# Performance work log

Measured on AMD Instinct MI355X. Metric: run time of the kernel, lower is better.

## Reference

```python
import jax, jax.numpy as jnp
import numpy as np

DELTA_VAR = 0.5
DELTA_DIST = 1.5
LOSS_WEIGHT = 1.0
L_MAX = 17  # segment ids 0..16 (0 = background)
EPS = 1e-12


def setup_inputs() -> dict:
    key = jax.random.key(0)
    k1, k2 = jax.random.split(key)
    B, D, H, W = 16, 16, 288, 512
    emb = jax.random.normal(k1, (B, D, H, W), dtype=jnp.float32)
    seg = jax.random.randint(k2, (B, 1, H, W), 0, L_MAX, dtype=jnp.int64)
    return {"input": emb, "target": seg}


def _per_image_losses(e, s):
    # e: [D, N] float, s: [N] int labels in [0, L_MAX)
    D, N = e.shape
    et = e.T  # [N, D]
    cnt = jax.ops.segment_sum(jnp.ones((N,), e.dtype), s, num_segments=L_MAX)  # [L]
    sums = jax.ops.segment_sum(et, s, num_segments=L_MAX)                      # [L, D]
    present = (cnt > 0) & (jnp.arange(L_MAX) != 0)
    num_lanes = jnp.sum(present).astype(e.dtype)
    means = sums / jnp.maximum(cnt, 1.0)[:, None]                              # [L, D]

    # variance (pull) term: per-pixel distance to own-label centroid
    diff = et - means[s]                                                       # [N, D]
    nrm = jnp.sqrt(jnp.maximum(jnp.sum(diff * diff, axis=1), EPS))             # [N]
    term = jax.nn.relu(nrm - DELTA_VAR) ** 2
    per_label = jax.ops.segment_sum(term, s, num_segments=L_MAX) / jnp.maximum(cnt, 1.0)
    var_l = jnp.sum(jnp.where(present, per_label, 0.0)) / jnp.maximum(num_lanes, 1.0)
    var_l = jnp.where(num_lanes > 0, var_l, 0.0)

    # distance (push) term: pairwise centroid distances among present lanes
    d = means[:, None, :] - means[None, :, :]                                  # [L, L, D]
    sumsq = jnp.sum(d * d, axis=2)                                             # [L, L]
    pair_mask = present[:, None] & present[None, :] & ~jnp.eye(L_MAX, dtype=bool)
    dist = jnp.sqrt(jnp.where(pair_mask, sumsq, 1.0))
    push = jnp.sum(jnp.where(pair_mask, jax.nn.relu(DELTA_DIST - dist) ** 2, 0.0))
    denom = jnp.maximum(num_lanes * (num_lanes - 1.0), 1.0)
    dist_l = jnp.where(num_lanes > 1, push / denom / 2.0, 0.0)
    return var_l, dist_l


def reference(input, target):
    B, D, H, W = input.shape
    N = H * W
    emb = input.reshape(B, D, N)
    seg = target.reshape(B, N).astype(jnp.int32)
    var_l, dist_l = jax.vmap(_per_image_losses)(emb, seg)
    loss = (jnp.sum(var_l) + jnp.sum(dist_l)) / B
    return loss * LOSS_WEIGHT
```

## Files before the change

### kernel.cpp

```cpp
#include <hip/hip_runtime.h>

#define BB   16
#define DD   16
#define NN   (288*512)
#define LL   17
#define TPB  256
#define PB   96
#define PXB  (NN/PB)
#define TILE 512
#define PBV  144
#define NREP 16

#define FSCALE 32768.0f
#define INV_FSCALE (1.0f/32768.0f)


__global__ __launch_bounds__(TPB) void k_accum(const float* __restrict__ emb,
                                               const int* __restrict__ seg,
                                               int* __restrict__ acc) {
    __shared__ int slab[TILE];
    __shared__ int tab[NREP * 289];
    const int tid  = threadIdx.x;
    const int b    = blockIdx.y;
    const int blk  = blockIdx.x;
    const int dgrp = tid >> 6;
    const int j    = tid & 63;
    int* trep = tab + (j & (NREP - 1)) * 289;

    for (int i = tid; i < NREP * 289; i += TPB) tab[i] = 0;

    const float* embb = emb + (size_t)b * DD * NN;
    const int*   segb = seg + (size_t)b * NN;
    const int base0 = blk * PXB;
    const float* r0 = embb + (size_t)(dgrp * 4 + 0) * NN;
    const float* r1 = embb + (size_t)(dgrp * 4 + 1) * NN;
    const float* r2 = embb + (size_t)(dgrp * 4 + 2) * NN;
    const float* r3 = embb + (size_t)(dgrp * 4 + 3) * NN;
    __syncthreads();

    for (int t = 0; t < PXB / TILE; ++t) {
        const int tb = base0 + t * TILE;
        if (tid < TILE / 4)
            *(int4*)(slab + tid * 4) = *(const int4*)(segb + tb + tid * 4);
        __syncthreads();
#pragma unroll
        for (int s = 0; s < TILE / 256; ++s) {
            const int p = s * 256 + j * 4;
            const int4   s4 = *(const int4*)(slab + p);
            const float4 e0 = *(const float4*)(r0 + tb + p);
            const float4 e1 = *(const float4*)(r1 + tb + p);
            const float4 e2 = *(const float4*)(r2 + tb + p);
            const float4 e3 = *(const float4*)(r3 + tb + p);
            const int o0 = s4.x * 17 + dgrp * 4;
            const int o1 = s4.y * 17 + dgrp * 4;
            const int o2 = s4.z * 17 + dgrp * 4;
            const int o3 = s4.w * 17 + dgrp * 4;
            atomicAdd(trep + o0 + 0, __float2int_rn(e0.x * FSCALE));
            atomicAdd(trep + o0 + 1, __float2int_rn(e1.x * FSCALE));
            atomicAdd(trep + o0 + 2, __float2int_rn(e2.x * FSCALE));
            atomicAdd(trep + o0 + 3, __float2int_rn(e3.x * FSCALE));
            atomicAdd(trep + o1 + 0, __float2int_rn(e0.y * FSCALE));
            atomicAdd(trep + o1 + 1, __float2int_rn(e1.y * FSCALE));
            atomicAdd(trep + o1 + 2, __float2int_rn(e2.y * FSCALE));
            atomicAdd(trep + o1 + 3, __float2int_rn(e3.y * FSCALE));
            atomicAdd(trep + o2 + 0, __float2int_rn(e0.z * FSCALE));
            atomicAdd(trep + o2 + 1, __float2int_rn(e1.z * FSCALE));
            atomicAdd(trep + o2 + 2, __float2int_rn(e2.z * FSCALE));
            atomicAdd(trep + o2 + 3, __float2int_rn(e3.z * FSCALE));
            atomicAdd(trep + o3 + 0, __float2int_rn(e0.w * FSCALE));
            atomicAdd(trep + o3 + 1, __float2int_rn(e1.w * FSCALE));
            atomicAdd(trep + o3 + 2, __float2int_rn(e2.w * FSCALE));
            atomicAdd(trep + o3 + 3, __float2int_rn(e3.w * FSCALE));
            if (dgrp == 0) {
                atomicAdd(trep + s4.x * 17 + 16, 1);
                atomicAdd(trep + s4.y * 17 + 16, 1);
                atomicAdd(trep + s4.z * 17 + 16, 1);
                atomicAdd(trep + s4.w * 17 + 16, 1);
            }
        }
        __syncthreads();
    }

    for (int i = tid; i < 289; i += TPB) {
        int v = 0;
#pragma unroll
        for (int r = 0; r < NREP; ++r) v += tab[r * 289 + i];
        atomicAdd(acc + b * 289 + i, v);
    }
}

__global__ __launch_bounds__(64) void k_stats(const int* __restrict__ acc,
                                              float* __restrict__ gmean,
                                              float* __restrict__ gw,
                                              float* __restrict__ dvec) {
    __shared__ float mm[289];
    const int tid = threadIdx.x;
    const int b = blockIdx.x;
    for (int i = tid; i < 289; i += 64) {
        const int raw = acc[b * 289 + i];
        mm[i] = (i % 17 == 16) ? (float)raw : (float)raw * INV_FSCALE;
    }
    __syncthreads();
    for (int i = tid; i < 272; i += 64) {
        const int l = i >> 4, d = i & 15;
        const float c = mm[l * 17 + 16];
        const float mv = mm[l * 17 + d] / fmaxf(c, 1.f);
        mm[l * 17 + d] = mv;
        gmean[(size_t)b * 272 + i] = mv;
    }
    __syncthreads();

    int nl = 0;
#pragma unroll
    for (int l = 1; l < LL; ++l) nl += (mm[l * 17 + 16] > 0.f) ? 1 : 0;
    const float nlf = (float)nl;

    if (tid < LL) {
        const bool pres = (tid != 0) && (mm[tid * 17 + 16] > 0.f);
        gw[(size_t)b * 17 + tid] = pres
            ? 1.f / (fmaxf(mm[tid * 17 + 16], 1.f) * fmaxf(nlf, 1.f) * (float)BB) : 0.f;
    }

    float push = 0.f;
    for (int p = tid; p < 289; p += 64) {
        const int i = p / 17, jj = p % 17;
        if (i != jj && i > 0 && jj > 0 && mm[i*17+16] > 0.f && mm[jj*17+16] > 0.f) {
            float ss = 0.f;
#pragma unroll
            for (int d = 0; d < DD; ++d) {
                const float df = mm[i*17+d] - mm[jj*17+d];
                ss += df * df;
            }
            const float t = fmaxf(1.5f - sqrtf(ss), 0.f);
            push += t * t;
        }
    }
#pragma unroll
    for (int off = 32; off; off >>= 1) push += __shfl_down(push, off, 64);
    if (tid == 0)
        dvec[b] = (nl > 1) ? push / (fmaxf(nlf * (nlf - 1.f), 1.f) * 2.f * (float)BB) : 0.f;
}

__global__ __launch_bounds__(TPB) void k_var(const float* __restrict__ emb,
                                             const int* __restrict__ seg,
                                             const float* __restrict__ gmean,
                                             const float* __restrict__ gw,
                                             float* __restrict__ vpart) {
    __shared__ float m[289];
    __shared__ float wl[17];
    __shared__ float wsum[TPB / 64];
    const int tid = threadIdx.x;
    const int b = blockIdx.y;
    for (int i = tid; i < 272; i += TPB)
        m[(i >> 4) * 17 + (i & 15)] = gmean[(size_t)b * 272 + i];
    if (tid < LL) wl[tid] = gw[(size_t)b * 17 + tid];
    __syncthreads();

    const float* embb = emb + (size_t)b * DD * NN;
    const int*   segb = seg + (size_t)b * NN;

    const int n = blockIdx.x * (TPB * 4) + tid * 4;
    const int4 s4 = *(const int4*)(segb + n);
    const int o0 = s4.x * 17, o1 = s4.y * 17, o2 = s4.z * 17, o3 = s4.w * 17;
    float ss0 = 0.f, ss1 = 0.f, ss2 = 0.f, ss3 = 0.f;
#pragma unroll
    for (int d = 0; d < DD; ++d) {
        const float4 e = *(const float4*)(embb + (size_t)d * NN + n);
        const float d0 = e.x - m[o0 + d]; ss0 += d0 * d0;
        const float d1 = e.y - m[o1 + d]; ss1 += d1 * d1;
        const float d2 = e.z - m[o2 + d]; ss2 += d2 * d2;
        const float d3 = e.w - m[o3 + d]; ss3 += d3 * d3;
    }
    float accl = 0.f, t;
    t = fmaxf(sqrtf(fmaxf(ss0, 1e-12f)) - 0.5f, 0.f); accl += t * t * wl[s4.x];
    t = fmaxf(sqrtf(fmaxf(ss1, 1e-12f)) - 0.5f, 0.f); accl += t * t * wl[s4.y];
    t = fmaxf(sqrtf(fmaxf(ss2, 1e-12f)) - 0.5f, 0.f); accl += t * t * wl[s4.z];
    t = fmaxf(sqrtf(fmaxf(ss3, 1e-12f)) - 0.5f, 0.f); accl += t * t * wl[s4.w];

#pragma unroll
    for (int off = 32; off; off >>= 1) accl += __shfl_down(accl, off, 64);
    if ((tid & 63) == 0) wsum[tid >> 6] = accl;
    __syncthreads();
    if (tid == 0)
        vpart[(size_t)b * PBV + blockIdx.x] = wsum[0] + wsum[1] + wsum[2] + wsum[3];
}

__global__ __launch_bounds__(TPB) void k_final(const float* __restrict__ vpart,
                                               const float* __restrict__ dvec,
                                               float* __restrict__ out) {
    __shared__ float ws4[TPB / 64];
    float v = 0.f;
    for (int i = threadIdx.x; i < BB * PBV; i += TPB) v += vpart[i];
    if (threadIdx.x < BB) v += dvec[threadIdx.x];
#pragma unroll
    for (int off = 32; off; off >>= 1) v += __shfl_down(v, off, 64);
    if ((threadIdx.x & 63) == 0) ws4[threadIdx.x >> 6] = v;
    __syncthreads();
    if (threadIdx.x == 0) out[0] = ws4[0] + ws4[1] + ws4[2] + ws4[3];
}

extern "C" void kernel_launch(void* const* d_in, const int* in_sizes, int n_in,
                              void* d_out, int out_size, void* d_ws, size_t ws_size,
                              hipStream_t stream) {
    const float* emb = (const float*)d_in[0];
    const int*   seg = (const int*)d_in[1];
    float* out = (float*)d_out;

    int*   acc   = (int*)d_ws;
    float* gmean = (float*)(acc + BB * 289);
    float* gw    = gmean + BB * 272;
    float* dvec  = gw + BB * 17;
    float* vpart = dvec + BB;

    hipMemsetAsync(acc, 0, (size_t)BB * 289 * sizeof(int), stream);

    k_accum<<<dim3(PB, BB), TPB, 0, stream>>>(emb, seg, acc);
    k_stats<<<BB, 64, 0, stream>>>(acc, gmean, gw, dvec);
    k_var  <<<dim3(PBV, BB), TPB, 0, stream>>>(emb, seg, gmean, gw, vpart);
    k_final<<<1, TPB, 0, stream>>>(vpart, dvec, out);
}
```

Measured before the change: 252.4 us.

## Fold stats kernel into variance kernel and drop shared seg staging

Removes the separate k_stats launch: each k_var block now recomputes the means and per-label weights from the integer accumulators, and block 0 of each image also computes the push term. k_accum loads segment labels straight from global memory instead of staging them in a shared slab, which removes the per-tile barriers. The shared replica count drops from 16 to 8. This cuts one launch and its serial dependency, at the cost of redundant per-block setup work and more LDS atomic contention with fewer replicas.

```diff
diff --git a/kernel.cpp b/kernel.cpp
--- a/kernel.cpp
+++ b/kernel.cpp
@@ -6,10 +6,9 @@
 #define LL   17
 #define TPB  256
 #define PB   96
-#define PXB  (NN/PB)
-#define TILE 512
+#define QB   (NN/4/PB)
 #define PBV  144
-#define NREP 16
+#define NREP 8
 
 #define FSCALE 32768.0f
 #define INV_FSCALE (1.0f/32768.0f)
@@ -18,7 +17,6 @@
 __global__ __launch_bounds__(TPB) void k_accum(const float* __restrict__ emb,
                                                const int* __restrict__ seg,
                                                int* __restrict__ acc) {
-    __shared__ int slab[TILE];
     __shared__ int tab[NREP * 289];
     const int tid  = threadIdx.x;
     const int b    = blockIdx.y;
@@ -31,55 +29,50 @@
 
     const float* embb = emb + (size_t)b * DD * NN;
     const int*   segb = seg + (size_t)b * NN;
-    const int base0 = blk * PXB;
     const float* r0 = embb + (size_t)(dgrp * 4 + 0) * NN;
     const float* r1 = embb + (size_t)(dgrp * 4 + 1) * NN;
     const float* r2 = embb + (size_t)(dgrp * 4 + 2) * NN;
     const float* r3 = embb + (size_t)(dgrp * 4 + 3) * NN;
+    const int q0 = blk * QB;
     __syncthreads();
 
-    for (int t = 0; t < PXB / TILE; ++t) {
-        const int tb = base0 + t * TILE;
-        if (tid < TILE / 4)
-            *(int4*)(slab + tid * 4) = *(const int4*)(segb + tb + tid * 4);
-        __syncthreads();
 #pragma unroll
-        for (int s = 0; s < TILE / 256; ++s) {
-            const int p = s * 256 + j * 4;
-            const int4   s4 = *(const int4*)(slab + p);
-            const float4 e0 = *(const float4*)(r0 + tb + p);
-            const float4 e1 = *(const float4*)(r1 + tb + p);
-            const float4 e2 = *(const float4*)(r2 + tb + p);
-            const float4 e3 = *(const float4*)(r3 + tb + p);
-            const int o0 = s4.x * 17 + dgrp * 4;
-            const int o1 = s4.y * 17 + dgrp * 4;
-            const int o2 = s4.z * 17 + dgrp * 4;
-            const int o3 = s4.w * 17 + dgrp * 4;
-            atomicAdd(trep + o0 + 0, __float2int_rn(e0.x * FSCALE));
-            atomicAdd(trep + o0 + 1, __float2int_rn(e1.x * FSCALE));
-            atomicAdd(trep + o0 + 2, __float2int_rn(e2.x * FSCALE));
-            atomicAdd(trep + o0 + 3, __float2int_rn(e3.x * FSCALE));
-            atomicAdd(trep + o1 + 0, __float2int_rn(e0.y * FSCALE));
-            atomicAdd(trep + o1 + 1, __float2int_rn(e1.y * FSCALE));
-            atomicAdd(trep + o1 + 2, __float2int_rn(e2.y * FSCALE));
-            atomicAdd(trep + o1 + 3, __float2int_rn(e3.y * FSCALE));
-            atomicAdd(trep + o2 + 0, __float2int_rn(e0.z * FSCALE));
-            atomicAdd(trep + o2 + 1, __float2int_rn(e1.z * FSCALE));
-            atomicAdd(trep + o2 + 2, __float2int_rn(e2.z * FSCALE));
-            atomicAdd(trep + o2 + 3, __float2int_rn(e3.z * FSCALE));
-            atomicAdd(trep + o3 + 0, __float2int_rn(e0.w * FSCALE));
-            atomicAdd(trep + o3 + 1, __float2int_rn(e1.w * FSCALE));
-            atomicAdd(trep + o3 + 2, __float2int_rn(e2.w * FSCALE));
-            atomicAdd(trep + o3 + 3, __float2int_rn(e3.w * FSCALE));
-            if (dgrp == 0) {
-                atomicAdd(trep + s4.x * 17 + 16, 1);
-                atomicAdd(trep + s4.y * 17 + 16, 1);
-                atomicAdd(trep + s4.z * 17 + 16, 1);
-                atomicAdd(trep + s4.w * 17 + 16, 1);
-            }
+    for (int it = 0; it < QB / 64; ++it) {
+        const int n = (q0 + it * 64 + j) * 4;
+        const int4   s4 = *(const int4*)(segb + n);
+        const float4 e0 = *(const float4*)(r0 + n);
+        const float4 e1 = *(const float4*)(r1 + n);
+        const float4 e2 = *(const float4*)(r2 + n);
+        const float4 e3 = *(const float4*)(r3 + n);
+        const int ch = dgrp * 4;
+        const int o0 = s4.x * 17 + ch;
+        const int o1 = s4.y * 17 + ch;
+        const int o2 = s4.z * 17 + ch;
+        const int o3 = s4.w * 17 + ch;
+        atomicAdd(trep + o0 + 0, __float2int_rn(e0.x * FSCALE));
+        atomicAdd(trep + o0 + 1, __float2int_rn(e1.x * FSCALE));
+        atomicAdd(trep + o0 + 2, __float2int_rn(e2.x * FSCALE));
+        atomicAdd(trep + o0 + 3, __float2int_rn(e3.x * FSCALE));
+        atomicAdd(trep + o1 + 0, __float2int_rn(e0.y * FSCALE));
+        atomicAdd(trep + o1 + 1, __float2int_rn(e1.y * FSCALE));
+        atomicAdd(trep + o1 + 2, __float2int_rn(e2.y * FSCALE));
+        atomicAdd(trep + o1 + 3, __float2int_rn(e3.y * FSCALE));
+        atomicAdd(trep + o2 + 0, __float2int_rn(e0.z * FSCALE));
+        atomicAdd(trep + o2 + 1, __float2int_rn(e1.z * FSCALE));
+        atomicAdd(trep + o2 + 2, __float2int_rn(e2.z * FSCALE));
+        atomicAdd(trep + o2 + 3, __float2int_rn(e3.z * FSCALE));
+        atomicAdd(trep + o3 + 0, __float2int_rn(e0.w * FSCALE));
+        atomicAdd(trep + o3 + 1, __float2int_rn(e1.w * FSCALE));
+        atomicAdd(trep + o3 + 2, __float2int_rn(e2.w * FSCALE));
+        atomicAdd(trep + o3 + 3, __float2int_rn(e3.w * FSCALE));
+        if (dgrp == 0) {
+            atomicAdd(trep + s4.x * 17 + 16, 1);
+            atomicAdd(trep + s4.y * 17 + 16, 1);
+            atomicAdd(trep + s4.z * 17 + 16, 1);
+            atomicAdd(trep + s4.w * 17 + 16, 1);
         }
-        __syncthreads();
     }
+    __syncthreads();
 
     for (int i = tid; i < 289; i += TPB) {
         int v = 0;
@@ -89,71 +82,36 @@
     }
 }
 
-__global__ __launch_bounds__(64) void k_stats(const int* __restrict__ acc,
-                                              float* __restrict__ gmean,
-                                              float* __restrict__ gw,
-                                              float* __restrict__ dvec) {
-    __shared__ float mm[289];
-    const int tid = threadIdx.x;
-    const int b = blockIdx.x;
-    for (int i = tid; i < 289; i += 64) {
-        const int raw = acc[b * 289 + i];
-        mm[i] = (i % 17 == 16) ? (float)raw : (float)raw * INV_FSCALE;
-    }
-    __syncthreads();
-    for (int i = tid; i < 272; i += 64) {
-        const int l = i >> 4, d = i & 15;
-        const float c = mm[l * 17 + 16];
-        const float mv = mm[l * 17 + d] / fmaxf(c, 1.f);
-        mm[l * 17 + d] = mv;
-        gmean[(size_t)b * 272 + i] = mv;
-    }
-    __syncthreads();
-
-    int nl = 0;
-#pragma unroll
-    for (int l = 1; l < LL; ++l) nl += (mm[l * 17 + 16] > 0.f) ? 1 : 0;
-    const float nlf = (float)nl;
-
-    if (tid < LL) {
-        const bool pres = (tid != 0) && (mm[tid * 17 + 16] > 0.f);
-        gw[(size_t)b * 17 + tid] = pres
-            ? 1.f / (fmaxf(mm[tid * 17 + 16], 1.f) * fmaxf(nlf, 1.f) * (float)BB) : 0.f;
-    }
-
-    float push = 0.f;
-    for (int p = tid; p < 289; p += 64) {
-        const int i = p / 17, jj = p % 17;
-        if (i != jj && i > 0 && jj > 0 && mm[i*17+16] > 0.f && mm[jj*17+16] > 0.f) {
-            float ss = 0.f;
-#pragma unroll
-            for (int d = 0; d < DD; ++d) {
-                const float df = mm[i*17+d] - mm[jj*17+d];
-                ss += df * df;
-            }
-            const float t = fmaxf(1.5f - sqrtf(ss), 0.f);
-            push += t * t;
-        }
-    }
-#pragma unroll
-    for (int off = 32; off; off >>= 1) push += __shfl_down(push, off, 64);
-    if (tid == 0)
-        dvec[b] = (nl > 1) ? push / (fmaxf(nlf * (nlf - 1.f), 1.f) * 2.f * (float)BB) : 0.f;
-}
-
 __global__ __launch_bounds__(TPB) void k_var(const float* __restrict__ emb,
                                              const int* __restrict__ seg,
-                                             const float* __restrict__ gmean,
-                                             const float* __restrict__ gw,
+                                             const int* __restrict__ acc,
                                              float* __restrict__ vpart) {
     __shared__ float m[289];
     __shared__ float wl[17];
     __shared__ float wsum[TPB / 64];
     const int tid = threadIdx.x;
     const int b = blockIdx.y;
-    for (int i = tid; i < 272; i += TPB)
-        m[(i >> 4) * 17 + (i & 15)] = gmean[(size_t)b * 272 + i];
-    if (tid < LL) wl[tid] = gw[(size_t)b * 17 + tid];
+
+    for (int i = tid; i < 289; i += TPB) {
+        const int raw = acc[b * 289 + i];
+        m[i] = (i % 17 == 16) ? (float)raw : (float)raw * INV_FSCALE;
+    }
+    __syncthreads();
+    for (int i = tid; i < 272; i += TPB) {
+        const int l = i >> 4, d = i & 15;
+        m[l * 17 + d] /= fmaxf(m[l * 17 + 16], 1.f);
+    }
+    __syncthreads();
+
+    int nl = 0;
+#pragma unroll
+    for (int l = 1; l < LL; ++l) nl += (m[l * 17 + 16] > 0.f) ? 1 : 0;
+    const float nlf = (float)nl;
+    if (tid < LL) {
+        const bool pres = (tid != 0) && (m[tid * 17 + 16] > 0.f);
+        wl[tid] = pres ? 1.f / (fmaxf(m[tid * 17 + 16], 1.f) * fmaxf(nlf, 1.f) * (float)BB)
+                       : 0.f;
+    }
     __syncthreads();
 
     const float* embb = emb + (size_t)b * DD * NN;
@@ -177,6 +135,24 @@
     t = fmaxf(sqrtf(fmaxf(ss2, 1e-12f)) - 0.5f, 0.f); accl += t * t * wl[s4.z];
     t = fmaxf(sqrtf(fmaxf(ss3, 1e-12f)) - 0.5f, 0.f); accl += t * t * wl[s4.w];
 
+    if (blockIdx.x == 0 && nl > 1) {
+        float push = 0.f;
+        for (int p = tid; p < 289; p += TPB) {
+            const int i = p / 17, jj = p % 17;
+            if (i != jj && i > 0 && jj > 0 && m[i*17+16] > 0.f && m[jj*17+16] > 0.f) {
+                float ss = 0.f;
+#pragma unroll
+                for (int d = 0; d < DD; ++d) {
+                    const float df = m[i*17+d] - m[jj*17+d];
+                    ss += df * df;
+                }
+                const float u = fmaxf(1.5f - sqrtf(ss), 0.f);
+                push += u * u;
+            }
+        }
+        accl += push / (fmaxf(nlf * (nlf - 1.f), 1.f) * 2.f * (float)BB);
+    }
+
 #pragma unroll
     for (int off = 32; off; off >>= 1) accl += __shfl_down(accl, off, 64);
     if ((tid & 63) == 0) wsum[tid >> 6] = accl;
@@ -186,12 +162,10 @@
 }
 
 __global__ __launch_bounds__(TPB) void k_final(const float* __restrict__ vpart,
-                                               const float* __restrict__ dvec,
                                                float* __restrict__ out) {
     __shared__ float ws4[TPB / 64];
     float v = 0.f;
     for (int i = threadIdx.x; i < BB * PBV; i += TPB) v += vpart[i];
-    if (threadIdx.x < BB) v += dvec[threadIdx.x];
 #pragma unroll
     for (int off = 32; off; off >>= 1) v += __shfl_down(v, off, 64);
     if ((threadIdx.x & 63) == 0) ws4[threadIdx.x >> 6] = v;
@@ -207,15 +181,11 @@
     float* out = (float*)d_out;
 
     int*   acc   = (int*)d_ws;
-    float* gmean = (float*)(acc + BB * 289);
-    float* gw    = gmean + BB * 272;
-    float* dvec  = gw + BB * 17;
-    float* vpart = dvec + BB;
+    float* vpart = (float*)(acc + BB * 289);
 
     hipMemsetAsync(acc, 0, (size_t)BB * 289 * sizeof(int), stream);
 
     k_accum<<<dim3(PB, BB), TPB, 0, stream>>>(emb, seg, acc);
-    k_stats<<<BB, 64, 0, stream>>>(acc, gmean, gw, dvec);
-    k_var  <<<dim3(PBV, BB), TPB, 0, stream>>>(emb, seg, gmean, gw, vpart);
-    k_final<<<1, TPB, 0, stream>>>(vpart, dvec, out);
+    k_var  <<<dim3(PBV, BB), TPB, 0, stream>>>(emb, seg, acc, vpart);
+    k_final<<<1, TPB, 0, stream>>>(vpart, out);
 }
```

After: 246.2 us. 1.03x faster.
